# Performance work log

Measured on AMD Instinct MI355X. Metric: run time of the kernel, lower is better.

## Reference

```python
import jax, jax.numpy as jnp
import numpy as np

D_MODEL = 1024
HEADS = 16
D_K = D_MODEL // HEADS
D_FF = 4096
EPS = 1e-6


def setup_inputs() -> dict:
    key = jax.random.key(0)
    ks = jax.random.split(key, 16)
    s = 1.0 / np.sqrt(D_MODEL)
    inp = {
        'x': jax.random.normal(ks[0], (4, 2048, D_MODEL), dtype=jnp.float32),
        'Wq': jax.random.normal(ks[1], (D_MODEL, D_MODEL), dtype=jnp.float32) * s,
        'bq': jnp.zeros((D_MODEL,), jnp.float32),
        'Wk': jax.random.normal(ks[2], (D_MODEL, D_MODEL), dtype=jnp.float32) * s,
        'bk': jnp.zeros((D_MODEL,), jnp.float32),
        'Wv': jax.random.normal(ks[3], (D_MODEL, D_MODEL), dtype=jnp.float32) * s,
        'bv': jnp.zeros((D_MODEL,), jnp.float32),
        'Wo': jax.random.normal(ks[4], (D_MODEL, D_MODEL), dtype=jnp.float32) * s,
        'bo': jnp.zeros((D_MODEL,), jnp.float32),
        'alpha1': jnp.ones((D_MODEL,), jnp.float32),
        'bias1': jnp.zeros((D_MODEL,), jnp.float32),
        'alpha2': jnp.ones((D_MODEL,), jnp.float32),
        'bias2': jnp.zeros((D_MODEL,), jnp.float32),
        'W1': jax.random.normal(ks[5], (D_MODEL, D_FF), dtype=jnp.float32) * s,
        'b1': jnp.zeros((D_FF,), jnp.float32),
        'W2': jax.random.normal(ks[6], (D_FF, D_MODEL), dtype=jnp.float32) * (1.0 / np.sqrt(D_FF)),
        'b2': jnp.zeros((D_MODEL,), jnp.float32),
    }
    return inp


def _residual_norm(x, residual, alpha, bias):
    # x = x + residual; norm with mean and UNBIASED std (torch x.std default),
    # eps added to std (not variance), affine alpha/bias. Dropout = identity (eval).
    s = x + residual
    mean = jnp.mean(s, axis=-1, keepdims=True)
    std = jnp.std(s, axis=-1, keepdims=True, ddof=1)
    return alpha * (s - mean) / (std + EPS) + bias


def _forward(x, Wq, bq, Wk, bk, Wv, bv, Wo, bo, alpha1, bias1, alpha2, bias2, W1, b1, W2, b2):
    B, S, D = x.shape
    # QKV projections and head split: (B, H, S, d_k)
    def split_heads(t):
        return t.reshape(B, S, HEADS, D_K).transpose(0, 2, 1, 3)
    Q = split_heads(x @ Wq + bq)
    K = split_heads(x @ Wk + bk)
    V = split_heads(x @ Wv + bv)
    # scaled dot-product attention (no mask, no dropout in eval)
    scores = jnp.einsum('bhqd,bhkd->bhqk', Q, K) / np.sqrt(D_K)
    weights = jax.nn.softmax(scores, axis=-1)
    attn = jnp.einsum('bhqk,bhkd->bhqd', weights, V)
    concat = attn.transpose(0, 2, 1, 3).reshape(B, S, D)
    attn_out = concat @ Wo + bo
    # post-norm residual 1
    norm1 = _residual_norm(attn_out, x, alpha1, bias1)
    # FFN (dropout = identity in eval)
    ff = jax.nn.relu(norm1 @ W1 + b1) @ W2 + b2
    # post-norm residual 2
    return _residual_norm(ff, norm1, alpha2, bias2)


def reference(x, Wq, bq, Wk, bk, Wv, bv, Wo, bo, alpha1, bias1, alpha2, bias2, W1, b1, W2, b2):
    return _forward(x, Wq, bq, Wk, bk, Wv, bv, Wo, bo, alpha1, bias1, alpha2, bias2, W1, b1, W2, b2)
```

## Files before the change

### kernel.cpp

```cpp
#include <hip/hip_runtime.h>
#include <hip/hip_bf16.h>
#include <stdint.h>

typedef __attribute__((ext_vector_type(8))) short bv8;
typedef __attribute__((ext_vector_type(4))) short sv4;
typedef __attribute__((ext_vector_type(4))) float f4;

#define LDS_AS __attribute__((address_space(3)))
#define GLB_AS __attribute__((address_space(1)))

#if __has_builtin(__builtin_amdgcn_exp2f)
#define EXP2F(x) __builtin_amdgcn_exp2f(x)
#else
#define EXP2F(x) exp2f(x)
#endif

__device__ __forceinline__ void gload16(const void* g, void* l) {
  __builtin_amdgcn_global_load_lds((GLB_AS void*)(g), (LDS_AS void*)(l), 16, 0, 0);
}

__device__ __forceinline__ short f2bs(float x) {
  return __builtin_bit_cast(short, __float2bfloat16(x));
}
__device__ __forceinline__ float bs2f(short s) {
  unsigned u = ((unsigned)(unsigned short)s) << 16;
  return __builtin_bit_cast(float, u);
}

__global__ __launch_bounds__(256) void k_cvt(const float* __restrict__ in, short* __restrict__ out) {
  const int i = (blockIdx.x * 256 + threadIdx.x) * 4;
  const float4 v = *(const float4*)(in + i);
  sv4 o; o[0] = f2bs(v.x); o[1] = f2bs(v.y); o[2] = f2bs(v.z); o[3] = f2bs(v.w);
  *(sv4*)(out + i) = o;
}

__global__ __launch_bounds__(256) void k_transpose(const float* __restrict__ W, short* __restrict__ Wt,
                                                   int K, int N) {
  __shared__ float tile[32][33];
  const int tx = threadIdx.x & 31, ty = threadIdx.x >> 5;
  const int n0 = blockIdx.x * 32, k0 = blockIdx.y * 32;
#pragma unroll
  for (int i = 0; i < 32; i += 8)
    tile[ty + i][tx] = W[(size_t)(k0 + ty + i) * N + n0 + tx];
  __syncthreads();
#pragma unroll
  for (int i = 0; i < 32; i += 8)
    Wt[(size_t)(n0 + ty + i) * K + k0 + tx] = f2bs(tile[tx][ty + i]);
}

template<int EPI>
__global__ __launch_bounds__(256) void k_gemm(const short* __restrict__ A, const short* __restrict__ Bt,
                                              const float* __restrict__ bias, short* __restrict__ C,
                                              int M, int N, int K) {
  __shared__ __align__(16) short As[128 * 64];
  __shared__ __align__(16) short Bs[128 * 64];
  const int t = threadIdx.x;
  const int lane = t & 63, w = t >> 6;
  const int wm = w >> 1, wn = w & 1;
  const int lr = lane & 15, lg = lane >> 4;
  const int m0 = blockIdx.y * 128, n0 = blockIdx.x * 128;

  f4 acc[4][4] = {};

  for (int k0 = 0; k0 < K; k0 += 64) {
    __syncthreads();
#pragma unroll
    for (int i = 0; i < 4; ++i) {
      const int L = t * 16 + i * 4096;
      const int row = L >> 7;
      const int cbs = (L & 127) ^ ((row & 7) << 4);
      gload16(A + (size_t)(m0 + row) * K + k0 + (cbs >> 1), (char*)As + L);
      gload16(Bt + (size_t)(n0 + row) * K + k0 + (cbs >> 1), (char*)Bs + L);
    }
    __syncthreads();
#pragma unroll
    for (int kk = 0; kk < 2; ++kk) {
      bv8 af[4], bfr[4];
#pragma unroll
      for (int mi = 0; mi < 4; ++mi) {
        const int row = wm * 64 + mi * 16 + lr;
        const int cb = kk * 64 + lg * 16;
        af[mi] = *(const bv8*)((const char*)As + row * 128 + (cb ^ ((row & 7) << 4)));
      }
#pragma unroll
      for (int ni = 0; ni < 4; ++ni) {
        const int row = wn * 64 + ni * 16 + lr;
        const int cb = kk * 64 + lg * 16;
        bfr[ni] = *(const bv8*)((const char*)Bs + row * 128 + (cb ^ ((row & 7) << 4)));
      }
#pragma unroll
      for (int mi = 0; mi < 4; ++mi)
#pragma unroll
        for (int ni = 0; ni < 4; ++ni)
          acc[mi][ni] = __builtin_amdgcn_mfma_f32_16x16x32_bf16(af[mi], bfr[ni], acc[mi][ni], 0, 0, 0);
    }
  }

#pragma unroll
  for (int ni = 0; ni < 4; ++ni) {
    const int c = n0 + wn * 64 + ni * 16 + lr;
    const float bvs = bias[c];
#pragma unroll
    for (int mi = 0; mi < 4; ++mi) {
#pragma unroll
      for (int j = 0; j < 4; ++j) {
        const int r = m0 + wm * 64 + mi * 16 + lg * 4 + j;
        float v = acc[mi][ni][j] + bvs;
        if (EPI == 1) v = fmaxf(v, 0.f);
        size_t off;
        if (EPI == 2) {
          const int b = r >> 11, s = r & 2047, h = c >> 6, d = c & 63;
          off = ((size_t)(b * 16 + h) * 2048 + s) * 64 + d;
        } else if (EPI == 3) {
          const int b = r >> 11, s = r & 2047, h = c >> 6, d = c & 63;
          off = ((size_t)(b * 16 + h) * 64 + d) * 2048 + s;
        } else {
          off = (size_t)r * N + c;
        }
        C[off] = f2bs(v);
      }
    }
  }
}

__global__ __launch_bounds__(256) void k_attn(const short* __restrict__ Qg, const short* __restrict__ Kg,
                                              const short* __restrict__ Vtg, short* __restrict__ Oc) {
  __shared__ __align__(16) short Ks[2][128 * 64];
  __shared__ __align__(16) short Ps[4][32 * 64];

  const int t = threadIdx.x, lane = t & 63, w = t >> 6;
  const int lr = lane & 15, lg = lane >> 4;
  const int bid = blockIdx.x;
  const int wid = (bid & 7) * 128 + (bid >> 3);
  const int q0 = (wid & 15) * 128;
  const int bh = wid >> 4;
  const int b = bh >> 4, h = bh & 15;
  const short* Qp = Qg + (size_t)bh * 2048 * 64;
  const short* Kp = Kg + (size_t)bh * 2048 * 64;
  const short* Vp = Vtg + (size_t)bh * 64 * 2048;

  bv8 qf[2][2];
#pragma unroll
  for (int mi = 0; mi < 2; ++mi)
#pragma unroll
    for (int kk = 0; kk < 2; ++kk)
      qf[mi][kk] = *(const bv8*)(Qp + (size_t)(q0 + w * 32 + mi * 16 + lr) * 64 + kk * 32 + lg * 8);

  f4 Oa[2][4] = {};
  float lsum[2] = {0.f, 0.f};
  const float SC = 0.125f * 1.44269504089f;
  short* Pw = (short*)Ps[w];

#pragma unroll
  for (int i = 0; i < 4; ++i) {
    const int L = t * 16 + i * 4096;
    const int row = L >> 7;
    const int cbs = (L & 127) ^ ((row & 7) << 4);
    gload16(Kp + (size_t)row * 64 + (cbs >> 1), (char*)Ks[0] + L);
  }
  __syncthreads();

  int cur = 0;
  for (int kt = 0; kt < 2048; kt += 128) {
    if (kt + 128 < 2048) {
#pragma unroll
      for (int i = 0; i < 4; ++i) {
        const int L = t * 16 + i * 4096;
        const int row = L >> 7;
        const int cbs = (L & 127) ^ ((row & 7) << 4);
        gload16(Kp + (size_t)(kt + 128 + row) * 64 + (cbs >> 1), (char*)Ks[cur ^ 1] + L);
      }
    }
    const char* Kb = (const char*)Ks[cur];

#pragma unroll
    for (int hf = 0; hf < 2; ++hf) {
      f4 Sa[2][4] = {};
#pragma unroll
      for (int kk = 0; kk < 2; ++kk) {
        bv8 kf[4];
#pragma unroll
        for (int nl = 0; nl < 4; ++nl) {
          const int row = (hf * 4 + nl) * 16 + lr;
          const int cb = kk * 64 + lg * 16;
          kf[nl] = *(const bv8*)(Kb + row * 128 + (cb ^ ((row & 7) << 4)));
        }
        __builtin_amdgcn_s_setprio(1);
#pragma unroll
        for (int mi = 0; mi < 2; ++mi)
#pragma unroll
          for (int nl = 0; nl < 4; ++nl)
            Sa[mi][nl] = __builtin_amdgcn_mfma_f32_16x16x32_bf16(kf[nl], qf[mi][kk], Sa[mi][nl], 0, 0, 0);
        __builtin_amdgcn_s_setprio(0);
      }

#pragma unroll
      for (int mi = 0; mi < 2; ++mi) {
        float rs = 0.f;
#pragma unroll
        for (int nl = 0; nl < 4; ++nl)
#pragma unroll
          for (int j = 0; j < 4; ++j) {
            const float p = EXP2F(Sa[mi][nl][j] * SC);
            Sa[mi][nl][j] = p;
            rs += p;
          }
        lsum[mi] += rs;
      }

#pragma unroll
      for (int mi = 0; mi < 2; ++mi)
#pragma unroll
        for (int nl = 0; nl < 4; ++nl) {
          const int q = mi * 16 + lr;
          const int cb = (nl * 32 + lg * 8) ^ ((q & 7) << 4);
          sv4 pk;
          pk[0] = f2bs(Sa[mi][nl][0]); pk[1] = f2bs(Sa[mi][nl][1]);
          pk[2] = f2bs(Sa[mi][nl][2]); pk[3] = f2bs(Sa[mi][nl][3]);
          *(sv4*)((char*)Pw + q * 128 + cb) = pk;
        }

#pragma unroll
      for (int k2 = 0; k2 < 2; ++k2) {
        bv8 vf[4], pf[2];
#pragma unroll
        for (int nO = 0; nO < 4; ++nO)
          vf[nO] = *(const bv8*)(Vp + (size_t)(nO * 16 + lr) * 2048 + kt + hf * 64 + k2 * 32 + lg * 8);
#pragma unroll
        for (int mi = 0; mi < 2; ++mi) {
          const int row = mi * 16 + lr;
          const int cb = (k2 * 64 + lg * 16) ^ ((row & 7) << 4);
          pf[mi] = *(const bv8*)((const char*)Pw + row * 128 + cb);
        }
        __builtin_amdgcn_s_setprio(1);
#pragma unroll
        for (int mi = 0; mi < 2; ++mi)
#pragma unroll
          for (int nO = 0; nO < 4; ++nO)
            Oa[mi][nO] = __builtin_amdgcn_mfma_f32_16x16x32_bf16(vf[nO], pf[mi], Oa[mi][nO], 0, 0, 0);
        __builtin_amdgcn_s_setprio(0);
      }
    }

    __syncthreads();
    cur ^= 1;
  }

#pragma unroll
  for (int mi = 0; mi < 2; ++mi) {
    lsum[mi] += __shfl_xor(lsum[mi], 16);
    lsum[mi] += __shfl_xor(lsum[mi], 32);
  }

#pragma unroll
  for (int mi = 0; mi < 2; ++mi) {
    const float inv = 1.f / lsum[mi];
    const int q = q0 + w * 32 + mi * 16 + lr;
#pragma unroll
    for (int nO = 0; nO < 4; ++nO) {
      sv4 o;
#pragma unroll
      for (int j = 0; j < 4; ++j) o[j] = f2bs(Oa[mi][nO][j] * inv);
      const int c = h * 64 + nO * 16 + lg * 4;
      *(sv4*)(Oc + ((size_t)b * 2048 + q) * 1024 + c) = o;
    }
  }
}

template<int MODE>
__global__ __launch_bounds__(256) void k_resnorm(const short* __restrict__ a, const void* __restrict__ res,
                                                 const float* __restrict__ alpha, const float* __restrict__ beta,
                                                 void* __restrict__ out) {
  const int row = blockIdx.x;
  const int t = threadIdx.x;
  const int lane = t & 63, w = t >> 6;
  const size_t base = (size_t)row * 1024;

  const sv4 av = *(const sv4*)(a + base + t * 4);
  float v[4];
  if (MODE == 0) {
    const float4 rv = *(const float4*)((const float*)res + base + t * 4);
    v[0] = bs2f(av[0]) + rv.x; v[1] = bs2f(av[1]) + rv.y;
    v[2] = bs2f(av[2]) + rv.z; v[3] = bs2f(av[3]) + rv.w;
  } else {
    const sv4 rv = *(const sv4*)((const short*)res + base + t * 4);
#pragma unroll
    for (int i = 0; i < 4; ++i) v[i] = bs2f(av[i]) + bs2f(rv[i]);
  }
  float s = v[0] + v[1] + v[2] + v[3];
  float sq = v[0] * v[0] + v[1] * v[1] + v[2] * v[2] + v[3] * v[3];
#pragma unroll
  for (int m = 1; m < 64; m <<= 1) { s += __shfl_xor(s, m); sq += __shfl_xor(sq, m); }
  __shared__ float red[8];
  if (lane == 0) { red[w] = s; red[w + 4] = sq; }
  __syncthreads();
  s = red[0] + red[1] + red[2] + red[3];
  sq = red[4] + red[5] + red[6] + red[7];
  const float mean = s * (1.f / 1024.f);
  const float var = (sq - 1024.f * mean * mean) * (1.f / 1023.f);
  const float inv = 1.f / (sqrtf(fmaxf(var, 0.f)) + 1e-6f);
  const float4 al = *(const float4*)(alpha + t * 4);
  const float4 be = *(const float4*)(beta + t * 4);
  float y[4];
  y[0] = al.x * (v[0] - mean) * inv + be.x;
  y[1] = al.y * (v[1] - mean) * inv + be.y;
  y[2] = al.z * (v[2] - mean) * inv + be.z;
  y[3] = al.w * (v[3] - mean) * inv + be.w;
  if (MODE == 0) {
    sv4 o; o[0] = f2bs(y[0]); o[1] = f2bs(y[1]); o[2] = f2bs(y[2]); o[3] = f2bs(y[3]);
    *(sv4*)((short*)out + base + t * 4) = o;
  } else {
    *(float4*)((float*)out + base + t * 4) = make_float4(y[0], y[1], y[2], y[3]);
  }
}

extern "C" void kernel_launch(void* const* d_in, const int* in_sizes, int n_in,
                              void* d_out, int out_size, void* d_ws, size_t ws_size,
                              hipStream_t stream) {
  const float* x   = (const float*)d_in[0];
  const float* Wq  = (const float*)d_in[1];
  const float* bq  = (const float*)d_in[2];
  const float* Wk  = (const float*)d_in[3];
  const float* bk  = (const float*)d_in[4];
  const float* Wv  = (const float*)d_in[5];
  const float* bv  = (const float*)d_in[6];
  const float* Wo  = (const float*)d_in[7];
  const float* bo  = (const float*)d_in[8];
  const float* al1 = (const float*)d_in[9];
  const float* bi1 = (const float*)d_in[10];
  const float* al2 = (const float*)d_in[11];
  const float* bi2 = (const float*)d_in[12];
  const float* W1  = (const float*)d_in[13];
  const float* b1  = (const float*)d_in[14];
  const float* W2  = (const float*)d_in[15];
  const float* b2  = (const float*)d_in[16];

  if (ws_size < (size_t)136 * 1024 * 1024) return;

  char* ws = (char*)d_ws;
  short* xb  = (short*)(ws);
  short* Qb  = (short*)(ws + (16ll << 20));
  short* Kb  = (short*)(ws + (32ll << 20));
  short* Vtb = (short*)(ws + (48ll << 20));
  short* Hb  = (short*)(ws);
  short* Wqt = (short*)(ws + (64ll << 20));
  short* Wkt = (short*)(ws + (66ll << 20));
  short* Wvt = (short*)(ws + (68ll << 20));
  short* Wot = (short*)(ws + (70ll << 20));
  short* W1t = (short*)(ws + (72ll << 20));
  short* W2t = (short*)(ws + (80ll << 20));
  short* Cc  = (short*)(ws + (88ll << 20));
  short* AOb = (short*)(ws + (104ll << 20));
  short* N1b = (short*)(ws + (120ll << 20));
  short* FFb = (short*)(ws + (104ll << 20));

  k_cvt<<<8192, 256, 0, stream>>>(x, xb);
  k_transpose<<<dim3(32, 32), 256, 0, stream>>>(Wq, Wqt, 1024, 1024);
  k_transpose<<<dim3(32, 32), 256, 0, stream>>>(Wk, Wkt, 1024, 1024);
  k_transpose<<<dim3(32, 32), 256, 0, stream>>>(Wv, Wvt, 1024, 1024);
  k_transpose<<<dim3(32, 32), 256, 0, stream>>>(Wo, Wot, 1024, 1024);
  k_transpose<<<dim3(128, 32), 256, 0, stream>>>(W1, W1t, 1024, 4096);
  k_transpose<<<dim3(32, 128), 256, 0, stream>>>(W2, W2t, 4096, 1024);

  k_gemm<2><<<dim3(8, 64), 256, 0, stream>>>(xb, Wqt, bq, Qb, 8192, 1024, 1024);
  k_gemm<2><<<dim3(8, 64), 256, 0, stream>>>(xb, Wkt, bk, Kb, 8192, 1024, 1024);
  k_gemm<3><<<dim3(8, 64), 256, 0, stream>>>(xb, Wvt, bv, Vtb, 8192, 1024, 1024);

  k_attn<<<1024, 256, 0, stream>>>(Qb, Kb, Vtb, Cc);

  k_gemm<0><<<dim3(8, 64), 256, 0, stream>>>(Cc, Wot, bo, AOb, 8192, 1024, 1024);
  k_resnorm<0><<<8192, 256, 0, stream>>>(AOb, x, al1, bi1, N1b);

  k_gemm<1><<<dim3(32, 64), 256, 0, stream>>>(N1b, W1t, b1, Hb, 8192, 4096, 1024);
  k_gemm<0><<<dim3(8, 64), 256, 0, stream>>>(Hb, W2t, b2, FFb, 8192, 1024, 4096);
  k_resnorm<1><<<8192, 256, 0, stream>>>(FFb, N1b, al2, bi2, (float*)d_out);
}
```

Measured before the change: 483.6 us.

## Fuse QKV projections into one GEMM and keep attention P in registers

Replaces the three separate Q/K/V projection GEMM launches with a single 24x64-block GEMM that reads concatenated transposed weights and scatters each output column block into the Q, K or transposed-V layout. This removes two launches and lets a single grid cover the fused N dimension. In attention, the probability tile is packed with v_cvt_pk_bf16_f32 and redistributed across lanes via cross-lane shuffles, replacing the LDS write/read round trip. The fused GEMM assumes Wqt/Wkt/Wvt sit contiguously in the workspace, and the shuffle pattern must exactly match the MFMA operand layout.

```diff
diff --git a/kernel.cpp b/kernel.cpp
--- a/kernel.cpp
+++ b/kernel.cpp
@@ -5,6 +5,7 @@
 typedef __attribute__((ext_vector_type(8))) short bv8;
 typedef __attribute__((ext_vector_type(4))) short sv4;
 typedef __attribute__((ext_vector_type(4))) float f4;
+typedef __attribute__((ext_vector_type(4))) unsigned uv4;
 
 #define LDS_AS __attribute__((address_space(3)))
 #define GLB_AS __attribute__((address_space(1)))
@@ -25,6 +26,11 @@
 __device__ __forceinline__ float bs2f(short s) {
   unsigned u = ((unsigned)(unsigned short)s) << 16;
   return __builtin_bit_cast(float, u);
+}
+__device__ __forceinline__ unsigned cvtpk(float lo, float hi) {
+  unsigned r;
+  asm("v_cvt_pk_bf16_f32 %0, %1, %2" : "=v"(r) : "v"(lo), "v"(hi));
+  return r;
 }
 
 __global__ __launch_bounds__(256) void k_cvt(const float* __restrict__ in, short* __restrict__ out) {
@@ -107,17 +113,78 @@
         const int r = m0 + wm * 64 + mi * 16 + lg * 4 + j;
         float v = acc[mi][ni][j] + bvs;
         if (EPI == 1) v = fmaxf(v, 0.f);
-        size_t off;
-        if (EPI == 2) {
-          const int b = r >> 11, s = r & 2047, h = c >> 6, d = c & 63;
-          off = ((size_t)(b * 16 + h) * 2048 + s) * 64 + d;
-        } else if (EPI == 3) {
-          const int b = r >> 11, s = r & 2047, h = c >> 6, d = c & 63;
-          off = ((size_t)(b * 16 + h) * 64 + d) * 2048 + s;
-        } else {
-          off = (size_t)r * N + c;
-        }
-        C[off] = f2bs(v);
+        C[(size_t)r * N + c] = f2bs(v);
+      }
+    }
+  }
+}
+
+__global__ __launch_bounds__(256) void k_gemmqkv(const short* __restrict__ A, const short* __restrict__ Bt,
+                                                 const float* __restrict__ bq, const float* __restrict__ bk,
+                                                 const float* __restrict__ bv,
+                                                 short* __restrict__ Qb, short* __restrict__ Kb,
+                                                 short* __restrict__ Vtb) {
+  __shared__ __align__(16) short As[128 * 64];
+  __shared__ __align__(16) short Bs[128 * 64];
+  const int K = 1024;
+  const int t = threadIdx.x;
+  const int lane = t & 63, w = t >> 6;
+  const int wm = w >> 1, wn = w & 1;
+  const int lr = lane & 15, lg = lane >> 4;
+  const int m0 = blockIdx.y * 128, n0 = blockIdx.x * 128;
+
+  f4 acc[4][4] = {};
+
+  for (int k0 = 0; k0 < K; k0 += 64) {
+    __syncthreads();
+#pragma unroll
+    for (int i = 0; i < 4; ++i) {
+      const int L = t * 16 + i * 4096;
+      const int row = L >> 7;
+      const int cbs = (L & 127) ^ ((row & 7) << 4);
+      gload16(A + (size_t)(m0 + row) * K + k0 + (cbs >> 1), (char*)As + L);
+      gload16(Bt + (size_t)(n0 + row) * K + k0 + (cbs >> 1), (char*)Bs + L);
+    }
+    __syncthreads();
+#pragma unroll
+    for (int kk = 0; kk < 2; ++kk) {
+      bv8 af[4], bfr[4];
+#pragma unroll
+      for (int mi = 0; mi < 4; ++mi) {
+        const int row = wm * 64 + mi * 16 + lr;
+        const int cb = kk * 64 + lg * 16;
+        af[mi] = *(const bv8*)((const char*)As + row * 128 + (cb ^ ((row & 7) << 4)));
+      }
+#pragma unroll
+      for (int ni = 0; ni < 4; ++ni) {
+        const int row = wn * 64 + ni * 16 + lr;
+        const int cb = kk * 64 + lg * 16;
+        bfr[ni] = *(const bv8*)((const char*)Bs + row * 128 + (cb ^ ((row & 7) << 4)));
+      }
+#pragma unroll
+      for (int mi = 0; mi < 4; ++mi)
+#pragma unroll
+        for (int ni = 0; ni < 4; ++ni)
+          acc[mi][ni] = __builtin_amdgcn_mfma_f32_16x16x32_bf16(af[mi], bfr[ni], acc[mi][ni], 0, 0, 0);
+    }
+  }
+
+#pragma unroll
+  for (int ni = 0; ni < 4; ++ni) {
+    const int c = n0 + wn * 64 + ni * 16 + lr;
+    const int sel = c >> 10, cc = c & 1023;
+    const float bvs = (sel == 0 ? bq : sel == 1 ? bk : bv)[cc];
+    const int h = cc >> 6, d = cc & 63;
+#pragma unroll
+    for (int mi = 0; mi < 4; ++mi) {
+#pragma unroll
+      for (int j = 0; j < 4; ++j) {
+        const int r = m0 + wm * 64 + mi * 16 + lg * 4 + j;
+        const float v = acc[mi][ni][j] + bvs;
+        const int bb = r >> 11, s = r & 2047;
+        if (sel == 0)      Qb[((size_t)(bb * 16 + h) * 2048 + s) * 64 + d] = f2bs(v);
+        else if (sel == 1) Kb[((size_t)(bb * 16 + h) * 2048 + s) * 64 + d] = f2bs(v);
+        else               Vtb[((size_t)(bb * 16 + h) * 64 + d) * 2048 + s] = f2bs(v);
       }
     }
   }
@@ -126,7 +193,6 @@
 __global__ __launch_bounds__(256) void k_attn(const short* __restrict__ Qg, const short* __restrict__ Kg,
                                               const short* __restrict__ Vtg, short* __restrict__ Oc) {
   __shared__ __align__(16) short Ks[2][128 * 64];
-  __shared__ __align__(16) short Ps[4][32 * 64];
 
   const int t = threadIdx.x, lane = t & 63, w = t >> 6;
   const int lr = lane & 15, lg = lane >> 4;
@@ -149,7 +215,8 @@
   f4 Oa[2][4] = {};
   float lsum[2] = {0.f, 0.f};
   const float SC = 0.125f * 1.44269504089f;
-  short* Pw = (short*)Ps[w];
+  const bool hi = lg >= 2;
+  const bool xx = (lg == 1) || (lg == 2);
 
 #pragma unroll
   for (int i = 0; i < 4; ++i) {
@@ -209,18 +276,6 @@
       }
 
 #pragma unroll
-      for (int mi = 0; mi < 2; ++mi)
-#pragma unroll
-        for (int nl = 0; nl < 4; ++nl) {
-          const int q = mi * 16 + lr;
-          const int cb = (nl * 32 + lg * 8) ^ ((q & 7) << 4);
-          sv4 pk;
-          pk[0] = f2bs(Sa[mi][nl][0]); pk[1] = f2bs(Sa[mi][nl][1]);
-          pk[2] = f2bs(Sa[mi][nl][2]); pk[3] = f2bs(Sa[mi][nl][3]);
-          *(sv4*)((char*)Pw + q * 128 + cb) = pk;
-        }
-
-#pragma unroll
       for (int k2 = 0; k2 < 2; ++k2) {
         bv8 vf[4], pf[2];
 #pragma unroll
@@ -228,9 +283,21 @@
           vf[nO] = *(const bv8*)(Vp + (size_t)(nO * 16 + lr) * 2048 + kt + hf * 64 + k2 * 32 + lg * 8);
 #pragma unroll
         for (int mi = 0; mi < 2; ++mi) {
-          const int row = mi * 16 + lr;
-          const int cb = (k2 * 64 + lg * 16) ^ ((row & 7) << 4);
-          pf[mi] = *(const bv8*)((const char*)Pw + row * 128 + cb);
+          const unsigned W0 = cvtpk(Sa[mi][2 * k2][0], Sa[mi][2 * k2][1]);
+          const unsigned W1 = cvtpk(Sa[mi][2 * k2][2], Sa[mi][2 * k2][3]);
+          const unsigned W2 = cvtpk(Sa[mi][2 * k2 + 1][0], Sa[mi][2 * k2 + 1][1]);
+          const unsigned W3 = cvtpk(Sa[mi][2 * k2 + 1][2], Sa[mi][2 * k2 + 1][3]);
+          const unsigned w0 = hi ? W2 : W0, w1 = hi ? W3 : W1;
+          const unsigned s0 = __shfl_xor(hi ? W0 : W2, 32);
+          const unsigned s1 = __shfl_xor(hi ? W1 : W3, 32);
+          const unsigned t0 = __shfl_xor(xx ? w0 : s0, 16);
+          const unsigned t1 = __shfl_xor(xx ? w1 : s1, 16);
+          uv4 u;
+          u[0] = (lg == 0) ? w0 : (lg == 2) ? s0 : t0;
+          u[1] = (lg == 0) ? w1 : (lg == 2) ? s1 : t1;
+          u[2] = (lg == 3) ? w0 : (lg == 1) ? s0 : t0;
+          u[3] = (lg == 3) ? w1 : (lg == 1) ? s1 : t1;
+          pf[mi] = __builtin_bit_cast(bv8, u);
         }
         __builtin_amdgcn_s_setprio(1);
 #pragma unroll
@@ -362,9 +429,7 @@
   k_transpose<<<dim3(128, 32), 256, 0, stream>>>(W1, W1t, 1024, 4096);
   k_transpose<<<dim3(32, 128), 256, 0, stream>>>(W2, W2t, 4096, 1024);
 
-  k_gemm<2><<<dim3(8, 64), 256, 0, stream>>>(xb, Wqt, bq, Qb, 8192, 1024, 1024);
-  k_gemm<2><<<dim3(8, 64), 256, 0, stream>>>(xb, Wkt, bk, Kb, 8192, 1024, 1024);
-  k_gemm<3><<<dim3(8, 64), 256, 0, stream>>>(xb, Wvt, bv, Vtb, 8192, 1024, 1024);
+  k_gemmqkv<<<dim3(24, 64), 256, 0, stream>>>(xb, Wqt, bq, bk, bv, Qb, Kb, Vtb);
 
   k_attn<<<1024, 256, 0, stream>>>(Qb, Kb, Vtb, Cc);
 
```

After: 480.6 us. About the same (-0.6%).

## Pipeline 256x128 GEMM with triple-buffered LDS, fuse QKV, register-shuffle attention P

Applied to the files above, without the earlier changes.

Replaces the 128x128 GEMM with a 512-thread, 256x128-tile kernel. It uses a three-stage global_load_lds ring buffer with vmcnt-based waits, raised priority around the MFMA blocks, and an XCD-aware block-index swizzle. The Q, K and V projections become a single launch over a concatenated N=3072 weight, with the epilogue routing each column range to its head-split or transposed output. In attention, the softmax probabilities are packed to bf16 with v_cvt_pk_bf16_f32 and rearranged through cross-lane shuffles instead of a round trip through LDS. Costs are much higher LDS use (about 144KB per block), which limits occupancy, plus extra shuffle and select instructions.

```diff
diff --git a/kernel.cpp b/kernel.cpp
--- a/kernel.cpp
+++ b/kernel.cpp
@@ -5,6 +5,7 @@
 typedef __attribute__((ext_vector_type(8))) short bv8;
 typedef __attribute__((ext_vector_type(4))) short sv4;
 typedef __attribute__((ext_vector_type(4))) float f4;
+typedef __attribute__((ext_vector_type(4))) unsigned uv4;
 
 #define LDS_AS __attribute__((address_space(3)))
 #define GLB_AS __attribute__((address_space(1)))
@@ -26,6 +27,11 @@
   unsigned u = ((unsigned)(unsigned short)s) << 16;
   return __builtin_bit_cast(float, u);
 }
+__device__ __forceinline__ unsigned cvtpk(float lo, float hi) {
+  unsigned r;
+  asm("v_cvt_pk_bf16_f32 %0, %1, %2" : "=v"(r) : "v"(lo), "v"(hi));
+  return r;
+}
 
 __global__ __launch_bounds__(256) void k_cvt(const float* __restrict__ in, short* __restrict__ out) {
   const int i = (blockIdx.x * 256 + threadIdx.x) * 4;
@@ -49,57 +55,107 @@
 }
 
 template<int EPI>
-__global__ __launch_bounds__(256) void k_gemm(const short* __restrict__ A, const short* __restrict__ Bt,
-                                              const float* __restrict__ bias, short* __restrict__ C,
-                                              int M, int N, int K) {
-  __shared__ __align__(16) short As[128 * 64];
-  __shared__ __align__(16) short Bs[128 * 64];
+__global__ __launch_bounds__(512) void k_gemm256(const short* __restrict__ A, const short* __restrict__ Bt,
+                                                 const float* __restrict__ bias, const float* __restrict__ bias2,
+                                                 const float* __restrict__ bias3,
+                                                 short* __restrict__ C, short* __restrict__ D2,
+                                                 short* __restrict__ D3,
+                                                 int M, int N, int K, int nbx) {
+  __shared__ __align__(16) short As[3][256 * 64];
+  __shared__ __align__(16) short Bs[3][128 * 64];
+
   const int t = threadIdx.x;
   const int lane = t & 63, w = t >> 6;
   const int wm = w >> 1, wn = w & 1;
   const int lr = lane & 15, lg = lane >> 4;
-  const int m0 = blockIdx.y * 128, n0 = blockIdx.x * 128;
-
-  f4 acc[4][4] = {};
-
-  for (int k0 = 0; k0 < K; k0 += 64) {
-    __syncthreads();
+  const int nwg = gridDim.x, cpx = nwg >> 3;
+  const int bid = blockIdx.x;
+  const int wid = (bid & 7) * cpx + (bid >> 3);
+  const int by = wid / nbx, bx = wid % nbx;
+  const int m0 = by * 256, n0 = bx * 128;
+  const int nt = K >> 6;
+
+  auto STAGE = [&](int k0, int bufi) {
+    char* ad = (char*)As[bufi];
+    char* bd = (char*)Bs[bufi];
 #pragma unroll
     for (int i = 0; i < 4; ++i) {
-      const int L = t * 16 + i * 4096;
+      const int L = t * 16 + i * 8192;
       const int row = L >> 7;
       const int cbs = (L & 127) ^ ((row & 7) << 4);
-      gload16(A + (size_t)(m0 + row) * K + k0 + (cbs >> 1), (char*)As + L);
-      gload16(Bt + (size_t)(n0 + row) * K + k0 + (cbs >> 1), (char*)Bs + L);
-    }
-    __syncthreads();
+      gload16(A + (size_t)(m0 + row) * K + k0 + (cbs >> 1), ad + L);
+    }
+#pragma unroll
+    for (int i = 0; i < 2; ++i) {
+      const int L = t * 16 + i * 8192;
+      const int row = L >> 7;
+      const int cbs = (L & 127) ^ ((row & 7) << 4);
+      gload16(Bt + (size_t)(n0 + row) * K + k0 + (cbs >> 1), bd + L);
+    }
+  };
+
+  f4 acc[4][4] = {};
+
+  STAGE(0, 0);
+  STAGE(64, 1);
+  asm volatile("s_waitcnt vmcnt(6)" ::: "memory");
+  __builtin_amdgcn_sched_barrier(0);
+  __builtin_amdgcn_s_barrier();
+  __builtin_amdgcn_sched_barrier(0);
+
+  int cur = 0;
+  for (int tt = 0; tt < nt; ++tt) {
+    if (tt + 2 < nt) {
+      int b2 = cur + 2; if (b2 >= 3) b2 -= 3;
+      STAGE((tt + 2) << 6, b2);
+    }
+    const char* Ab = (const char*)As[cur];
+    const char* Bb = (const char*)Bs[cur];
 #pragma unroll
     for (int kk = 0; kk < 2; ++kk) {
-      bv8 af[4], bfr[4];
+      bv8 af[4], bf[4];
 #pragma unroll
       for (int mi = 0; mi < 4; ++mi) {
         const int row = wm * 64 + mi * 16 + lr;
         const int cb = kk * 64 + lg * 16;
-        af[mi] = *(const bv8*)((const char*)As + row * 128 + (cb ^ ((row & 7) << 4)));
+        af[mi] = *(const bv8*)(Ab + row * 128 + (cb ^ ((row & 7) << 4)));
       }
 #pragma unroll
       for (int ni = 0; ni < 4; ++ni) {
         const int row = wn * 64 + ni * 16 + lr;
         const int cb = kk * 64 + lg * 16;
-        bfr[ni] = *(const bv8*)((const char*)Bs + row * 128 + (cb ^ ((row & 7) << 4)));
-      }
+        bf[ni] = *(const bv8*)(Bb + row * 128 + (cb ^ ((row & 7) << 4)));
+      }
+      __builtin_amdgcn_s_setprio(1);
 #pragma unroll
       for (int mi = 0; mi < 4; ++mi)
 #pragma unroll
         for (int ni = 0; ni < 4; ++ni)
-          acc[mi][ni] = __builtin_amdgcn_mfma_f32_16x16x32_bf16(af[mi], bfr[ni], acc[mi][ni], 0, 0, 0);
-    }
+          acc[mi][ni] = __builtin_amdgcn_mfma_f32_16x16x32_bf16(af[mi], bf[ni], acc[mi][ni], 0, 0, 0);
+      __builtin_amdgcn_s_setprio(0);
+    }
+    if (tt + 1 < nt) {
+      if (tt + 2 < nt) asm volatile("s_waitcnt vmcnt(6)" ::: "memory");
+      else             asm volatile("s_waitcnt vmcnt(0)" ::: "memory");
+      __builtin_amdgcn_sched_barrier(0);
+      __builtin_amdgcn_s_barrier();
+      __builtin_amdgcn_sched_barrier(0);
+    }
+    cur += 1; if (cur >= 3) cur -= 3;
   }
 
 #pragma unroll
   for (int ni = 0; ni < 4; ++ni) {
     const int c = n0 + wn * 64 + ni * 16 + lr;
-    const float bvs = bias[c];
+    float bvs;
+    int sel = 0, cc = c, h = 0, d = 0;
+    if (EPI == 2) {
+      sel = c >> 10; cc = c & 1023;
+      bvs = (sel == 0 ? bias : sel == 1 ? bias2 : bias3)[cc];
+      h = cc >> 6; d = cc & 63;
+    } else {
+      bvs = bias[c];
+    }
 #pragma unroll
     for (int mi = 0; mi < 4; ++mi) {
 #pragma unroll
@@ -107,17 +163,14 @@
         const int r = m0 + wm * 64 + mi * 16 + lg * 4 + j;
         float v = acc[mi][ni][j] + bvs;
         if (EPI == 1) v = fmaxf(v, 0.f);
-        size_t off;
         if (EPI == 2) {
-          const int b = r >> 11, s = r & 2047, h = c >> 6, d = c & 63;
-          off = ((size_t)(b * 16 + h) * 2048 + s) * 64 + d;
-        } else if (EPI == 3) {
-          const int b = r >> 11, s = r & 2047, h = c >> 6, d = c & 63;
-          off = ((size_t)(b * 16 + h) * 64 + d) * 2048 + s;
+          const int bb = r >> 11, s = r & 2047;
+          if (sel == 0)      C [((size_t)(bb * 16 + h) * 2048 + s) * 64 + d] = f2bs(v);
+          else if (sel == 1) D2[((size_t)(bb * 16 + h) * 2048 + s) * 64 + d] = f2bs(v);
+          else               D3[((size_t)(bb * 16 + h) * 64 + d) * 2048 + s] = f2bs(v);
         } else {
-          off = (size_t)r * N + c;
+          C[(size_t)r * N + c] = f2bs(v);
         }
-        C[off] = f2bs(v);
       }
     }
   }
@@ -126,7 +179,6 @@
 __global__ __launch_bounds__(256) void k_attn(const short* __restrict__ Qg, const short* __restrict__ Kg,
                                               const short* __restrict__ Vtg, short* __restrict__ Oc) {
   __shared__ __align__(16) short Ks[2][128 * 64];
-  __shared__ __align__(16) short Ps[4][32 * 64];
 
   const int t = threadIdx.x, lane = t & 63, w = t >> 6;
   const int lr = lane & 15, lg = lane >> 4;
@@ -149,7 +201,8 @@
   f4 Oa[2][4] = {};
   float lsum[2] = {0.f, 0.f};
   const float SC = 0.125f * 1.44269504089f;
-  short* Pw = (short*)Ps[w];
+  const bool hi = lg >= 2;
+  const bool xx = (lg == 1) || (lg == 2);
 
 #pragma unroll
   for (int i = 0; i < 4; ++i) {
@@ -209,18 +262,6 @@
       }
 
 #pragma unroll
-      for (int mi = 0; mi < 2; ++mi)
-#pragma unroll
-        for (int nl = 0; nl < 4; ++nl) {
-          const int q = mi * 16 + lr;
-          const int cb = (nl * 32 + lg * 8) ^ ((q & 7) << 4);
-          sv4 pk;
-          pk[0] = f2bs(Sa[mi][nl][0]); pk[1] = f2bs(Sa[mi][nl][1]);
-          pk[2] = f2bs(Sa[mi][nl][2]); pk[3] = f2bs(Sa[mi][nl][3]);
-          *(sv4*)((char*)Pw + q * 128 + cb) = pk;
-        }
-
-#pragma unroll
       for (int k2 = 0; k2 < 2; ++k2) {
         bv8 vf[4], pf[2];
 #pragma unroll
@@ -228,9 +269,21 @@
           vf[nO] = *(const bv8*)(Vp + (size_t)(nO * 16 + lr) * 2048 + kt + hf * 64 + k2 * 32 + lg * 8);
 #pragma unroll
         for (int mi = 0; mi < 2; ++mi) {
-          const int row = mi * 16 + lr;
-          const int cb = (k2 * 64 + lg * 16) ^ ((row & 7) << 4);
-          pf[mi] = *(const bv8*)((const char*)Pw + row * 128 + cb);
+          const unsigned W0 = cvtpk(Sa[mi][2 * k2][0], Sa[mi][2 * k2][1]);
+          const unsigned W1 = cvtpk(Sa[mi][2 * k2][2], Sa[mi][2 * k2][3]);
+          const unsigned W2 = cvtpk(Sa[mi][2 * k2 + 1][0], Sa[mi][2 * k2 + 1][1]);
+          const unsigned W3 = cvtpk(Sa[mi][2 * k2 + 1][2], Sa[mi][2 * k2 + 1][3]);
+          const unsigned w0 = hi ? W2 : W0, w1 = hi ? W3 : W1;
+          const unsigned s0 = __shfl_xor(hi ? W0 : W2, 32);
+          const unsigned s1 = __shfl_xor(hi ? W1 : W3, 32);
+          const unsigned t0 = __shfl_xor(xx ? w0 : s0, 16);
+          const unsigned t1 = __shfl_xor(xx ? w1 : s1, 16);
+          uv4 u;
+          u[0] = (lg == 0) ? w0 : (lg == 2) ? s0 : t0;
+          u[1] = (lg == 0) ? w1 : (lg == 2) ? s1 : t1;
+          u[2] = (lg == 3) ? w0 : (lg == 1) ? s0 : t0;
+          u[3] = (lg == 3) ? w1 : (lg == 1) ? s1 : t1;
+          pf[mi] = __builtin_bit_cast(bv8, u);
         }
         __builtin_amdgcn_s_setprio(1);
 #pragma unroll
@@ -362,16 +415,17 @@
   k_transpose<<<dim3(128, 32), 256, 0, stream>>>(W1, W1t, 1024, 4096);
   k_transpose<<<dim3(32, 128), 256, 0, stream>>>(W2, W2t, 4096, 1024);
 
-  k_gemm<2><<<dim3(8, 64), 256, 0, stream>>>(xb, Wqt, bq, Qb, 8192, 1024, 1024);
-  k_gemm<2><<<dim3(8, 64), 256, 0, stream>>>(xb, Wkt, bk, Kb, 8192, 1024, 1024);
-  k_gemm<3><<<dim3(8, 64), 256, 0, stream>>>(xb, Wvt, bv, Vtb, 8192, 1024, 1024);
+  k_gemm256<2><<<768, 512, 0, stream>>>(xb, Wqt, bq, bk, bv, Qb, Kb, Vtb, 8192, 3072, 1024, 24);
 
   k_attn<<<1024, 256, 0, stream>>>(Qb, Kb, Vtb, Cc);
 
-  k_gemm<0><<<dim3(8, 64), 256, 0, stream>>>(Cc, Wot, bo, AOb, 8192, 1024, 1024);
+  k_gemm256<0><<<256, 512, 0, stream>>>(Cc, Wot, bo, nullptr, nullptr, AOb, nullptr, nullptr,
+                                        8192, 1024, 1024, 8);
   k_resnorm<0><<<8192, 256, 0, stream>>>(AOb, x, al1, bi1, N1b);
 
-  k_gemm<1><<<dim3(32, 64), 256, 0, stream>>>(N1b, W1t, b1, Hb, 8192, 4096, 1024);
-  k_gemm<0><<<dim3(8, 64), 256, 0, stream>>>(Hb, W2t, b2, FFb, 8192, 1024, 4096);
+  k_gemm256<1><<<1024, 512, 0, stream>>>(N1b, W1t, b1, nullptr, nullptr, Hb, nullptr, nullptr,
+                                         8192, 4096, 1024, 32);
+  k_gemm256<0><<<256, 512, 0, stream>>>(Hb, W2t, b2, nullptr, nullptr, FFb, nullptr, nullptr,
+                                        8192, 1024, 4096, 8);
   k_resnorm<1><<<8192, 256, 0, stream>>>(FFb, N1b, al2, bi2, (float*)d_out);
 }
```

New measurement: 505.4 us. 1.05x slower.
